# Kernel optimization log

Hardware: AMD Instinct MI355X
Metric: run time of the kernel (lower is better)

Reference implementation:

```python
import jax, jax.numpy as jnp
import numpy as np
import math

ALPHA, BETA, GAMMA = 12.0, 24.0, 96.0  # alpha=12, beta=2a, gamma=8a
PIX_PER_PATCH = 12.0                    # 200 // 16
HEADS = 8


def _bucket_ids(ct):
    # ct: (B,T,2) -> pairwise euclidean distance, trunc-divided by pix_per_patch
    d = ct[:, :, None, :] - ct[:, None, :, :]
    dist = jnp.trunc(jnp.sqrt(jnp.sum(d * d, axis=-1)) / PIX_PER_PATCH)
    absd = jnp.abs(dist)
    safe = jnp.maximum(absd, ALPHA)  # avoid log(0) in non-selected branch
    log_branch = jnp.sign(dist) * jnp.minimum(
        BETA, jnp.round(ALPHA + jnp.log(safe / ALPHA) / math.log(GAMMA / ALPHA) * (BETA - ALPHA)))
    # piecewise_index: identity (truncated to int) inside [-alpha, alpha], log-spaced outside
    idx = jnp.where(absd <= ALPHA, dist, log_branch).astype(jnp.int32) + int(BETA)
    return idx  # (B,T,T), values in [0, 2*beta]


def reference(x, ct, W_attn, b_attn, W_proj, b_proj, lut_bias):
    B, T, _ = x.shape
    H = HEADS
    n_embd = W_proj.shape[0]
    hd = n_embd // H
    idx = _bucket_ids(ct)

    qkv = x @ W_attn + b_attn                 # (B,T,3*n_embd)
    q, k, v = jnp.split(qkv, 3, axis=-1)
    q = q.reshape(B, T, H, hd).transpose(0, 2, 1, 3)  # (B,H,T,hd)
    k = k.reshape(B, T, H, hd).transpose(0, 2, 1, 3)
    v = v.reshape(B, T, H, hd).transpose(0, 2, 1, 3)

    att = jnp.einsum('bhtd,bhsd->bhts', q, k) / math.sqrt(hd)  # (B,H,T,T)
    # mask buffer is all-ones in the original, so masked_fill is a no-op.
    # Faithful to torch: gather (H, B*T*T) then raw row-major view to (B,H,T,T)
    rpe = lut_bias[:, idx.reshape(-1)].reshape(B, H, T, T)
    att = jax.nn.softmax(att + rpe, axis=-1)

    y = jnp.einsum('bhts,bhsd->bhtd', att, v)  # (B,H,T,hd)
    y = y.transpose(0, 2, 1, 3).reshape(B, T, n_embd)
    return y @ W_proj + b_proj


def setup_inputs() -> dict:
    B, T, IN_C, N_EMBD, NB = 16, 500, 512, 512, 49
    key = jax.random.key(0)
    ks = jax.random.split(key, 7)
    s = 0.02
    return {
        'x': jax.random.normal(ks[0], (B, T, IN_C), jnp.float32),
        'ct': jax.random.uniform(ks[1], (B, T, 2), jnp.float32) * 200.0,
        'W_attn': jax.random.normal(ks[2], (IN_C, 3 * N_EMBD), jnp.float32) * s,
        'b_attn': jax.random.normal(ks[3], (3 * N_EMBD,), jnp.float32) * s,
        'W_proj': jax.random.normal(ks[4], (N_EMBD, N_EMBD), jnp.float32) * s,
        'b_proj': jax.random.normal(ks[5], (N_EMBD,), jnp.float32) * s,
        'lut_bias': jax.random.normal(ks[6], (HEADS, NB), jnp.float32) * s,
    }
```

## Files before the change

### kernel.cpp

```cpp
#include <hip/hip_runtime.h>
#include <hip/hip_bf16.h>

typedef __bf16 bf16;
typedef __bf16 bf16x4 __attribute__((ext_vector_type(4)));
typedef __bf16 bf16x8 __attribute__((ext_vector_type(8)));
typedef float  f32x4  __attribute__((ext_vector_type(4)));

#define MFMA(a, b, c) __builtin_amdgcn_mfma_f32_16x16x32_bf16((a), (b), (c), 0, 0, 0)

__device__ __forceinline__ void async_ld16(void* l, const void* g) {
    __builtin_amdgcn_global_load_lds(
        (const __attribute__((address_space(1))) void*)g,
        (__attribute__((address_space(3))) void*)l, 16, 0, 0);
}


__global__ void cvt_f32_bf16(const float4* __restrict__ src, ushort4* __restrict__ dst, int n4) {
    for (int i = blockIdx.x * blockDim.x + threadIdx.x; i < n4; i += gridDim.x * blockDim.x) {
        float4 v = src[i];
        ushort4 o;
        o.x = (unsigned short)(__bfloat16_as_ushort(__float2bfloat16(v.x)));
        o.y = (unsigned short)(__bfloat16_as_ushort(__float2bfloat16(v.y)));
        o.z = (unsigned short)(__bfloat16_as_ushort(__float2bfloat16(v.z)));
        o.w = (unsigned short)(__bfloat16_as_ushort(__float2bfloat16(v.w)));
        dst[i] = o;
    }
}

__global__ void transpose_f32_bf16(const float* __restrict__ src, bf16* __restrict__ dst,
                                   int K, int N) {
    int i = blockIdx.x * 256 + threadIdx.x;
    if (i < K * N) {
        int k = i / N, n = i % N;
        dst[n * K + k] = (bf16)src[i];
    }
}

__global__ void pad_zero(bf16* __restrict__ xb, bf16* __restrict__ yb,
                         bf16* __restrict__ qb, bf16* __restrict__ kbuf,
                         bf16* __restrict__ vtb) {
    const bf16x8 z8 = {(bf16)0.f, (bf16)0.f, (bf16)0.f, (bf16)0.f,
                       (bf16)0.f, (bf16)0.f, (bf16)0.f, (bf16)0.f};
    const bf16x4 z4 = {(bf16)0.f, (bf16)0.f, (bf16)0.f, (bf16)0.f};
    int i = blockIdx.x * 256 + threadIdx.x;
    if (i < 4096) {
        *(bf16x8*)(xb + (size_t)8000 * 512 + i * 8) = z8;
    } else if (i < 8192) {
        *(bf16x8*)(yb + (size_t)8000 * 512 + (i - 4096) * 8) = z8;
    } else if (i < 20480) {
        int c = i - 8192;
        int bh = c / 96, rem = c % 96;
        int t = 500 + rem / 8, d8 = rem % 8;
        *(bf16x8*)(qb + (((size_t)bh * 512 + t) * 64) + d8 * 8) = z8;
    } else if (i < 32768) {
        int c = i - 20480;
        int bh = c / 96, rem = c % 96;
        int t = 500 + rem / 8, d8 = rem % 8;
        *(bf16x8*)(kbuf + (((size_t)bh * 512 + t) * 64) + d8 * 8) = z8;
    } else if (i < 40960) {
        int w = i - 32768;
        int bh = w >> 6, d = w & 63;
        bf16* base = vtb + ((size_t)bh * 64 + d) * 512 + 500;
        *(bf16x4*)base = z4;
        *(bf16x8*)(base + 4) = z8;
    }
}

__global__ void bucket_kernel(const float* __restrict__ ct, unsigned char* __restrict__ idx) {
    const int b = blockIdx.x >> 9;
    const int t = blockIdx.x & 511;
    const bool tv = (t < 500);
    float ctx = 0.f, cty = 0.f;
    if (tv) {
        ctx = ct[(b * 500 + t) * 2];
        cty = ct[(b * 500 + t) * 2 + 1];
    }
    const int s0 = threadIdx.x * 4;
    uchar4 o;
    unsigned char v[4];
#pragma unroll
    for (int j = 0; j < 4; j++) {
        int s = s0 + j;
        unsigned char r = 63;
        if (tv && s < 500) {
            float dx = ctx - ct[(b * 500 + s) * 2];
            float dy = cty - ct[(b * 500 + s) * 2 + 1];
            float dist = truncf(sqrtf(dx * dx + dy * dy) / 12.0f);
            int bi;
            if (dist <= 12.0f) {
                bi = (int)dist;
            } else {
                float lb = fminf(24.0f, rintf(12.0f + (logf(dist / 12.0f) * (1.0f / 2.0794415416798357f)) * 12.0f));
                bi = (int)lb;
            }
            r = (unsigned char)(bi + 24);
        }
        v[j] = r;
    }
    o.x = v[0]; o.y = v[1]; o.z = v[2]; o.w = v[3];
    *(uchar4*)(idx + ((size_t)blockIdx.x) * 512 + s0) = o;
}

template<int BN, int WGM, int WGN, int EPI>
__global__ __launch_bounds__(256) void gemm128(const bf16* __restrict__ A,
                                               const bf16* __restrict__ Bt,
                                               const float* __restrict__ bias,
                                               bf16* __restrict__ o_q,
                                               bf16* __restrict__ o_k,
                                               bf16* __restrict__ o_v,
                                               float* __restrict__ o_f) {
    constexpr int BM = 128, BK = 64, K = 512, NT = K / BK;
    constexpr int WM = BM / (WGM * 16);
    constexpr int WN = BN / (WGN * 16);
    constexpr int NA = BM * 8 / 256;
    constexpr int NB = BN * 8 / 256;
    constexpr int LD = (BM + BN) * BK;

    __shared__ __align__(1024) bf16 lds[2 * LD];

    const int lane = threadIdx.x & 63;
    const int wave = threadIdx.x >> 6;

    const int gdx = gridDim.x;
    const int nwg = gdx * gridDim.y;
    const int bid = blockIdx.y * gdx + blockIdx.x;
    const int qq = nwg >> 3, rr = nwg & 7;
    const int xcd = bid & 7, jj = bid >> 3;
    const int wg = (xcd < rr ? xcd * (qq + 1) : rr * (qq + 1) + (xcd - rr) * qq) + jj;
    const int m0 = (wg / gdx) * BM;
    const int n0 = (wg % gdx) * BN;

    const int wr = wave / WGN, wc = wave % WGN;
    const int r = lane & 15, g = lane >> 4;

    const bf16* pa[NA];
    const bf16* pb[NB];
    int loA[NA], loB[NB];
#pragma unroll
    for (int i = 0; i < NA; i++) {
        int cbase = i * 256 + wave * 64;
        int c = cbase + lane;
        int row = c >> 3, cb = (c & 7) * 16;
        pa[i] = A + (size_t)(m0 + row) * K + ((cb ^ ((row & 7) << 4)) >> 1);
        loA[i] = cbase * 8;
    }
#pragma unroll
    for (int i = 0; i < NB; i++) {
        int cbase = i * 256 + wave * 64;
        int c = cbase + lane;
        int row = c >> 3, cb = (c & 7) * 16;
        pb[i] = Bt + (size_t)(n0 + row) * K + ((cb ^ ((row & 7) << 4)) >> 1);
        loB[i] = cbase * 8;
    }

    f32x4 acc[WM][WN];
#pragma unroll
    for (int i = 0; i < WM; i++)
#pragma unroll
        for (int j = 0; j < WN; j++) acc[i][j] = (f32x4){0.f, 0.f, 0.f, 0.f};

    auto stage = [&](int buf, int kt) {
        bf16* la = lds + buf * LD;
        bf16* lb = la + BM * BK;
#pragma unroll
        for (int i = 0; i < NA; i++) async_ld16(la + loA[i], pa[i] + kt);
#pragma unroll
        for (int i = 0; i < NB; i++) async_ld16(lb + loB[i], pb[i] + kt);
    };

    stage(0, 0);
    int cur = 0;
#pragma unroll
    for (int t = 0; t < NT; t++) {
        if (t + 1 < NT) {
            stage(cur ^ 1, (t + 1) * BK);
            asm volatile("s_waitcnt vmcnt(%0)" ::"i"(NA + NB) : "memory");
        } else {
            asm volatile("s_waitcnt vmcnt(0)" ::: "memory");
        }
        __builtin_amdgcn_s_barrier();
        const bf16* la = lds + cur * LD;
        const bf16* lb = la + BM * BK;
#pragma unroll
        for (int kh = 0; kh < 2; kh++) {
            const int cb = kh * 64 + g * 16;
            bf16x8 af[WM], bfv[WN];
#pragma unroll
            for (int mf = 0; mf < WM; mf++) {
                int fr = wr * WM * 16 + mf * 16 + r;
                af[mf] = *(const bf16x8*)&la[fr * 64 + ((cb ^ ((fr & 7) << 4)) >> 1)];
            }
#pragma unroll
            for (int nf = 0; nf < WN; nf++) {
                int fr = wc * WN * 16 + nf * 16 + r;
                bfv[nf] = *(const bf16x8*)&lb[fr * 64 + ((cb ^ ((fr & 7) << 4)) >> 1)];
            }
#pragma unroll
            for (int mf = 0; mf < WM; mf++)
#pragma unroll
                for (int nf = 0; nf < WN; nf++)
                    acc[mf][nf] = MFMA(af[mf], bfv[nf], acc[mf][nf]);
        }
        asm volatile("" ::: "memory");
        __builtin_amdgcn_s_barrier();
        cur ^= 1;
    }

    if (EPI == 0) {
        const bool isv = (n0 >= 1024);
        bf16* tile = lds;
#pragma unroll
        for (int mf = 0; mf < WM; mf++)
#pragma unroll
            for (int nf = 0; nf < WN; nf++) {
                int nl = wc * WN * 16 + nf * 16 + r;
                float bv = bias[n0 + nl];
#pragma unroll
                for (int reg = 0; reg < 4; reg++) {
                    int ml = wr * WM * 16 + mf * 16 + g * 4 + reg;
                    bf16 val = (bf16)(acc[mf][nf][reg] + bv);
                    int byte = isv ? (nl * 256 + ((ml * 2) ^ ((nl & 7) << 4)))
                                   : (ml * 256 + ((nl * 2) ^ ((ml & 7) << 4)));
                    tile[byte >> 1] = val;
                }
            }
        __syncthreads();
        const int h0 = (n0 & 511) >> 6;
        if (!isv) {
            bf16* dst = (n0 < 512) ? o_q : o_k;
#pragma unroll
            for (int j = 0; j < 8; j++) {
                int seg = wave * 64 + j * 8 + (lane >> 3);
                int ml = seg >> 1, hp = seg & 1;
                int m = m0 + ml;
                if (m < 8000) {
                    int cb2 = (hp * 128 + (lane & 7) * 16) ^ ((ml & 7) << 4);
                    bf16x8 v8 = *(const bf16x8*)&tile[(ml * 256 + cb2) >> 1];
                    int b = m / 500, t = m - b * 500;
                    *(bf16x8*)&dst[(((size_t)(b * 8 + h0 + hp)) * 512 + t) * 64 + (lane & 7) * 8] = v8;
                }
            }
        } else {
#pragma unroll
            for (int j = 0; j < 8; j++) {
                int seg = wave * 64 + j * 8 + (lane >> 3);
                int nl = seg >> 1, mh = seg & 1;
                int mloc = mh * 64 + (lane & 7) * 8;
                int m = m0 + mloc;
                if (m < 8000) {
                    int cb2 = (mh * 128 + (lane & 7) * 16) ^ ((nl & 7) << 4);
                    bf16x8 v8 = *(const bf16x8*)&tile[(nl * 256 + cb2) >> 1];
                    int h = h0 + (nl >> 6), d = nl & 63;
                    int b0 = m / 500, b1 = (m + 7) / 500;
                    if (b0 == b1) {
                        int t = m - b0 * 500;
                        bf16* p = o_v + (((size_t)(b0 * 8 + h)) * 64 + d) * 512 + t;
                        if ((t & 7) == 0) {
                            *(bf16x8*)p = v8;
                        } else {
                            bf16x4 lo = {v8[0], v8[1], v8[2], v8[3]};
                            bf16x4 hi = {v8[4], v8[5], v8[6], v8[7]};
                            *(bf16x4*)p = lo;
                            *(bf16x4*)(p + 4) = hi;
                        }
                    } else {
#pragma unroll
                        for (int i = 0; i < 8; i++) {
                            int mi = m + i;
                            int bb = mi / 500, tt = mi - bb * 500;
                            o_v[(((size_t)(bb * 8 + h)) * 64 + d) * 512 + tt] = v8[i];
                        }
                    }
                }
            }
        }
    } else {
#pragma unroll
        for (int mf = 0; mf < WM; mf++) {
#pragma unroll
            for (int nf = 0; nf < WN; nf++) {
                int n = n0 + wc * WN * 16 + nf * 16 + r;
                float bv = bias[n];
#pragma unroll
                for (int reg = 0; reg < 4; reg++) {
                    int m = m0 + wr * WM * 16 + mf * 16 + g * 4 + reg;
                    if (m < 8000) o_f[(size_t)m * 512 + n] = acc[mf][nf][reg] + bv;
                }
            }
        }
    }
}

__global__ __launch_bounds__(256) void attn_kernel(const bf16* __restrict__ qb,
                                                   const bf16* __restrict__ kbuf,
                                                   const bf16* __restrict__ vtb,
                                                   const unsigned char* __restrict__ idxg,
                                                   const float* __restrict__ lut,
                                                   bf16* __restrict__ yb) {
    __shared__ __align__(1024) bf16 KT[2][4096];
    __shared__ __align__(1024) bf16 VT[2][4096];
    __shared__ float lut_s[64];
    __shared__ __align__(16) bf16 P[4][2][16][72];

    const int lane = threadIdx.x & 63;
    const int wave = threadIdx.x >> 6;
    const int tid = threadIdx.x;
    const int bid0 = blockIdx.x;
    const int wg = (bid0 & 7) * 64 + (bid0 >> 3);
    const int bh = wg >> 2;
    const int qt = wg & 3;
    const int b = bh >> 3;
    const int h = bh & 7;

    if (tid < 64)
        lut_s[tid] = (tid < 49) ? lut[h * 49 + tid] * 1.4426950408889634f : -1e30f;

    const int r = lane & 15;
    const int g = lane >> 4;
    const int ko = g << 3;
    const int rowbase = qt * 128 + wave * 32;

    bf16x8 qf[2][2];
#pragma unroll
    for (int c = 0; c < 2; c++) {
        const bf16* qp = qb + ((size_t)bh * 512 + rowbase + c * 16 + r) * 64 + ko;
        qf[c][0] = *(const bf16x8*)qp;
        qf[c][1] = *(const bf16x8*)(qp + 32);
    }

    const bf16* kbb = kbuf + (size_t)bh * 512 * 64;
    const bf16* vbb = vtb + (size_t)bh * 64 * 512;
    const unsigned char* ip0 = idxg + ((size_t)b * 512 + rowbase + r) * 512;
    const unsigned char* ip1 = ip0 + (size_t)16 * 512;

    const int c0 = tid, c1 = 256 + tid;
    const int kr0 = c0 >> 3, ks0 = (c0 & 7) * 16;
    const int kr1 = c1 >> 3, ks1 = (c1 & 7) * 16;
    const bf16* ksrc0 = kbb + (size_t)kr0 * 64 + ((ks0 ^ ((kr0 & 7) << 4)) >> 1);
    const bf16* ksrc1 = kbb + (size_t)kr1 * 64 + ((ks1 ^ ((kr1 & 7) << 4)) >> 1);
    const bf16* vsrc0 = vbb + (size_t)kr0 * 512 + ((ks0 ^ ((kr0 & 7) << 4)) >> 1);
    const bf16* vsrc1 = vbb + (size_t)kr1 * 512 + ((ks1 ^ ((kr1 & 7) << 4)) >> 1);

    auto stage = [&](int buf, int s0) {
        async_ld16(&KT[buf][c0 * 8], ksrc0 + (size_t)s0 * 64);
        async_ld16(&KT[buf][c1 * 8], ksrc1 + (size_t)s0 * 64);
        async_ld16(&VT[buf][c0 * 8], vsrc0 + s0);
        async_ld16(&VT[buf][c1 * 8], vsrc1 + s0);
    };

    unsigned int idb[2][2][4];
    auto ldidx = [&](int par, int s0) {
#pragma unroll
        for (int nf = 0; nf < 4; nf++) {
            idb[par][0][nf] = *(const unsigned int*)(ip0 + s0 + nf * 16 + (g << 2));
            idb[par][1][nf] = *(const unsigned int*)(ip1 + s0 + nf * 16 + (g << 2));
        }
    };

    f32x4 o[2][4];
#pragma unroll
    for (int c = 0; c < 2; c++)
#pragma unroll
        for (int i = 0; i < 4; i++) o[c][i] = (f32x4){0.f, 0.f, 0.f, 0.f};
    float lsum[2] = {0.f, 0.f};

    const float QS = 0.125f * 1.4426950408889634f;

    stage(0, 0);
    ldidx(0, 0);
#pragma unroll
    for (int ti = 0; ti < 8; ti++) {
        const int buf = ti & 1;
        const int s0 = ti * 64;
        if (ti < 7) {
            stage(buf ^ 1, s0 + 64);
            ldidx((ti + 1) & 1, s0 + 64);
            asm volatile("s_waitcnt vmcnt(12)" ::: "memory");
        } else {
            asm volatile("s_waitcnt vmcnt(0)" ::: "memory");
        }
        __builtin_amdgcn_s_barrier();
        f32x4 sa[2][4];
        __builtin_amdgcn_s_setprio(1);
#pragma unroll
        for (int nf = 0; nf < 4; nf++) {
            const int row = nf * 16 + r;
            const int swz = (row & 7) << 4;
            bf16x8 kf0 = *(const bf16x8*)&KT[buf][row * 64 + (((g * 16) ^ swz) >> 1)];
            bf16x8 kf1 = *(const bf16x8*)&KT[buf][row * 64 + (((g * 16 + 64) ^ swz) >> 1)];
            sa[0][nf] = MFMA(kf0, qf[0][0], ((f32x4){0.f, 0.f, 0.f, 0.f}));
            sa[0][nf] = MFMA(kf1, qf[0][1], sa[0][nf]);
            sa[1][nf] = MFMA(kf0, qf[1][0], ((f32x4){0.f, 0.f, 0.f, 0.f}));
            sa[1][nf] = MFMA(kf1, qf[1][1], sa[1][nf]);
        }
        __builtin_amdgcn_s_setprio(0);
#pragma unroll
        for (int c = 0; c < 2; c++) {
            float ts = 0.f;
#pragma unroll
            for (int nf = 0; nf < 4; nf++) {
                unsigned int u = idb[ti & 1][c][nf];
                float p0 = exp2f(fmaf(sa[c][nf][0], QS, lut_s[u & 255]));
                float p1 = exp2f(fmaf(sa[c][nf][1], QS, lut_s[(u >> 8) & 255]));
                float p2 = exp2f(fmaf(sa[c][nf][2], QS, lut_s[(u >> 16) & 255]));
                float p3 = exp2f(fmaf(sa[c][nf][3], QS, lut_s[u >> 24]));
                ts += (p0 + p1) + (p2 + p3);
                bf16x4 pk = {(bf16)p0, (bf16)p1, (bf16)p2, (bf16)p3};
                *(bf16x4*)&P[wave][c][r][nf * 16 + (g << 2)] = pk;
            }
            lsum[c] += ts;
        }
        bf16x8 pf00 = *(const bf16x8*)&P[wave][0][r][ko];
        bf16x8 pf01 = *(const bf16x8*)&P[wave][0][r][32 + ko];
        bf16x8 pf10 = *(const bf16x8*)&P[wave][1][r][ko];
        bf16x8 pf11 = *(const bf16x8*)&P[wave][1][r][32 + ko];
        __builtin_amdgcn_s_setprio(1);
#pragma unroll
        for (int nf = 0; nf < 4; nf++) {
            const int row = nf * 16 + r;
            const int swz = (row & 7) << 4;
            bf16x8 vf0 = *(const bf16x8*)&VT[buf][row * 64 + (((g * 16) ^ swz) >> 1)];
            bf16x8 vf1 = *(const bf16x8*)&VT[buf][row * 64 + (((g * 16 + 64) ^ swz) >> 1)];
            o[0][nf] = MFMA(pf00, vf0, o[0][nf]);
            o[0][nf] = MFMA(pf01, vf1, o[0][nf]);
            o[1][nf] = MFMA(pf10, vf0, o[1][nf]);
            o[1][nf] = MFMA(pf11, vf1, o[1][nf]);
        }
        __builtin_amdgcn_s_setprio(0);
        asm volatile("" ::: "memory");
        __builtin_amdgcn_s_barrier();
    }
#pragma unroll
    for (int c = 0; c < 2; c++) {
        float ls = lsum[c];
        ls += __shfl_xor(ls, 16);
        ls += __shfl_xor(ls, 32);
        float invl = 1.0f / ls;
#pragma unroll
        for (int reg = 0; reg < 4; reg++) {
            float il = __shfl(invl, (g << 2) + reg);
            int t = rowbase + c * 16 + (g << 2) + reg;
            if (t < 500) {
                bf16* yp = yb + ((size_t)(b * 500 + t)) * 512 + h * 64;
#pragma unroll
                for (int nf = 0; nf < 4; nf++) yp[nf * 16 + r] = (bf16)(o[c][nf][reg] * il);
            }
        }
    }
}

extern "C" void kernel_launch(void* const* d_in, const int* in_sizes, int n_in,
                              void* d_out, int out_size, void* d_ws, size_t ws_size,
                              hipStream_t stream) {
    const float* x     = (const float*)d_in[0];
    const float* ct    = (const float*)d_in[1];
    const float* Wattn = (const float*)d_in[2];
    const float* battn = (const float*)d_in[3];
    const float* Wproj = (const float*)d_in[4];
    const float* bproj = (const float*)d_in[5];
    const float* lut   = (const float*)d_in[6];
    float* out = (float*)d_out;

    char* w = (char*)d_ws;
    bf16* xb   = (bf16*)w;                w += (size_t)8064 * 512 * 2;
    bf16* Wa_t = (bf16*)w;                w += (size_t)1536 * 512 * 2;
    bf16* Wp_t = (bf16*)w;                w += (size_t)512 * 512 * 2;
    bf16* qb   = (bf16*)w;                w += (size_t)16 * 8 * 512 * 64 * 2;
    bf16* kbuf = (bf16*)w;                w += (size_t)16 * 8 * 512 * 64 * 2;
    bf16* vtb  = (bf16*)w;                w += (size_t)16 * 8 * 64 * 512 * 2;
    unsigned char* idxb = (unsigned char*)w; w += (size_t)16 * 512 * 512;
    bf16* yb   = (bf16*)w;                w += (size_t)8064 * 512 * 2;

    cvt_f32_bf16<<<dim3(2048), 256, 0, stream>>>((const float4*)x, (ushort4*)xb, (8000 * 512) / 4);
    transpose_f32_bf16<<<dim3((512 * 1536 + 255) / 256), 256, 0, stream>>>(Wattn, Wa_t, 512, 1536);
    transpose_f32_bf16<<<dim3((512 * 512 + 255) / 256), 256, 0, stream>>>(Wproj, Wp_t, 512, 512);
    pad_zero<<<dim3(160), 256, 0, stream>>>(xb, yb, qb, kbuf, vtb);
    bucket_kernel<<<dim3(16 * 512), 128, 0, stream>>>(ct, idxb);

    gemm128<128, 2, 2, 0><<<dim3(12, 63), 256, 0, stream>>>(xb, Wa_t, battn, qb, kbuf, vtb, nullptr);

    attn_kernel<<<dim3(512), 256, 0, stream>>>(qb, kbuf, vtb, idxb, lut, yb);

    gemm128<64, 4, 1, 1><<<dim3(8, 63), 256, 0, stream>>>(yb, Wp_t, bproj, nullptr, nullptr, nullptr, out);
}
```

Before: 93.02 us.

## Double KV tile to 128 keys and reorder barrier before prefetch in attention

```diff
diff --git a/kernel.cpp b/kernel.cpp
--- a/kernel.cpp
+++ b/kernel.cpp
@@ -297,8 +297,8 @@
                                                    const unsigned char* __restrict__ idxg,
                                                    const float* __restrict__ lut,
                                                    bf16* __restrict__ yb) {
-    __shared__ __align__(1024) bf16 KT[2][4096];
-    __shared__ __align__(1024) bf16 VT[2][4096];
+    __shared__ __align__(1024) bf16 KT[2][8192];
+    __shared__ __align__(1024) bf16 VT[2][8192];
     __shared__ float lut_s[64];
     __shared__ __align__(16) bf16 P[4][2][16][72];
 
@@ -330,31 +330,37 @@
 
     const bf16* kbb = kbuf + (size_t)bh * 512 * 64;
     const bf16* vbb = vtb + (size_t)bh * 64 * 512;
+
+    const bf16* ksrc[4];
+    const bf16* vsrc[4];
+    int loC[4];
+#pragma unroll
+    for (int i = 0; i < 4; i++) {
+        int c = i * 256 + tid;
+        loC[i] = c * 8;
+        int kr = c >> 3, ks = (c & 7) * 16;
+        ksrc[i] = kbb + (size_t)kr * 64 + ((ks ^ ((kr & 7) << 4)) >> 1);
+        int vr = c >> 4, vs = (c & 15) * 16;
+        vsrc[i] = vbb + (size_t)vr * 512 + ((vs ^ ((vr & 7) << 4)) >> 1);
+    }
+    auto stage = [&](int buf, int s0) {
+#pragma unroll
+        for (int i = 0; i < 4; i++) async_ld16(&KT[buf][loC[i]], ksrc[i] + (size_t)s0 * 64);
+#pragma unroll
+        for (int i = 0; i < 4; i++) async_ld16(&VT[buf][loC[i]], vsrc[i] + s0);
+    };
+
     const unsigned char* ip0 = idxg + ((size_t)b * 512 + rowbase + r) * 512;
     const unsigned char* ip1 = ip0 + (size_t)16 * 512;
-
-    const int c0 = tid, c1 = 256 + tid;
-    const int kr0 = c0 >> 3, ks0 = (c0 & 7) * 16;
-    const int kr1 = c1 >> 3, ks1 = (c1 & 7) * 16;
-    const bf16* ksrc0 = kbb + (size_t)kr0 * 64 + ((ks0 ^ ((kr0 & 7) << 4)) >> 1);
-    const bf16* ksrc1 = kbb + (size_t)kr1 * 64 + ((ks1 ^ ((kr1 & 7) << 4)) >> 1);
-    const bf16* vsrc0 = vbb + (size_t)kr0 * 512 + ((ks0 ^ ((kr0 & 7) << 4)) >> 1);
-    const bf16* vsrc1 = vbb + (size_t)kr1 * 512 + ((ks1 ^ ((kr1 & 7) << 4)) >> 1);
-
-    auto stage = [&](int buf, int s0) {
-        async_ld16(&KT[buf][c0 * 8], ksrc0 + (size_t)s0 * 64);
-        async_ld16(&KT[buf][c1 * 8], ksrc1 + (size_t)s0 * 64);
-        async_ld16(&VT[buf][c0 * 8], vsrc0 + s0);
-        async_ld16(&VT[buf][c1 * 8], vsrc1 + s0);
-    };
-
-    unsigned int idb[2][2][4];
+    unsigned int idb[2][2][2][4];
     auto ldidx = [&](int par, int s0) {
 #pragma unroll
-        for (int nf = 0; nf < 4; nf++) {
-            idb[par][0][nf] = *(const unsigned int*)(ip0 + s0 + nf * 16 + (g << 2));
-            idb[par][1][nf] = *(const unsigned int*)(ip1 + s0 + nf * 16 + (g << 2));
-        }
+        for (int sub = 0; sub < 2; sub++)
+#pragma unroll
+            for (int nf = 0; nf < 4; nf++) {
+                idb[par][sub][0][nf] = *(const unsigned int*)(ip0 + s0 + sub * 64 + nf * 16 + (g << 2));
+                idb[par][sub][1][nf] = *(const unsigned int*)(ip1 + s0 + sub * 64 + nf * 16 + (g << 2));
+            }
     };
 
     f32x4 o[2][4];
@@ -369,66 +375,65 @@
     stage(0, 0);
     ldidx(0, 0);
 #pragma unroll
-    for (int ti = 0; ti < 8; ti++) {
-        const int buf = ti & 1;
-        const int s0 = ti * 64;
-        if (ti < 7) {
-            stage(buf ^ 1, s0 + 64);
-            ldidx((ti + 1) & 1, s0 + 64);
-            asm volatile("s_waitcnt vmcnt(12)" ::: "memory");
-        } else {
-            asm volatile("s_waitcnt vmcnt(0)" ::: "memory");
-        }
+    for (int it = 0; it < 4; it++) {
+        const int buf = it & 1;
+        const int s0 = it * 128;
+        asm volatile("s_waitcnt vmcnt(0)" ::: "memory");
         __builtin_amdgcn_s_barrier();
-        f32x4 sa[2][4];
-        __builtin_amdgcn_s_setprio(1);
-#pragma unroll
-        for (int nf = 0; nf < 4; nf++) {
-            const int row = nf * 16 + r;
-            const int swz = (row & 7) << 4;
-            bf16x8 kf0 = *(const bf16x8*)&KT[buf][row * 64 + (((g * 16) ^ swz) >> 1)];
-            bf16x8 kf1 = *(const bf16x8*)&KT[buf][row * 64 + (((g * 16 + 64) ^ swz) >> 1)];
-            sa[0][nf] = MFMA(kf0, qf[0][0], ((f32x4){0.f, 0.f, 0.f, 0.f}));
-            sa[0][nf] = MFMA(kf1, qf[0][1], sa[0][nf]);
-            sa[1][nf] = MFMA(kf0, qf[1][0], ((f32x4){0.f, 0.f, 0.f, 0.f}));
-            sa[1][nf] = MFMA(kf1, qf[1][1], sa[1][nf]);
-        }
-        __builtin_amdgcn_s_setprio(0);
-#pragma unroll
-        for (int c = 0; c < 2; c++) {
-            float ts = 0.f;
+        if (it < 3) {
+            stage(buf ^ 1, s0 + 128);
+            ldidx((it + 1) & 1, s0 + 128);
+        }
+#pragma unroll
+        for (int sub = 0; sub < 2; sub++) {
+            f32x4 sa[2][4];
+            __builtin_amdgcn_s_setprio(1);
 #pragma unroll
             for (int nf = 0; nf < 4; nf++) {
-                unsigned int u = idb[ti & 1][c][nf];
-                float p0 = exp2f(fmaf(sa[c][nf][0], QS, lut_s[u & 255]));
-                float p1 = exp2f(fmaf(sa[c][nf][1], QS, lut_s[(u >> 8) & 255]));
-                float p2 = exp2f(fmaf(sa[c][nf][2], QS, lut_s[(u >> 16) & 255]));
-                float p3 = exp2f(fmaf(sa[c][nf][3], QS, lut_s[u >> 24]));
-                ts += (p0 + p1) + (p2 + p3);
-                bf16x4 pk = {(bf16)p0, (bf16)p1, (bf16)p2, (bf16)p3};
-                *(bf16x4*)&P[wave][c][r][nf * 16 + (g << 2)] = pk;
-            }
-            lsum[c] += ts;
-        }
-        bf16x8 pf00 = *(const bf16x8*)&P[wave][0][r][ko];
-        bf16x8 pf01 = *(const bf16x8*)&P[wave][0][r][32 + ko];
-        bf16x8 pf10 = *(const bf16x8*)&P[wave][1][r][ko];
-        bf16x8 pf11 = *(const bf16x8*)&P[wave][1][r][32 + ko];
-        __builtin_amdgcn_s_setprio(1);
-#pragma unroll
-        for (int nf = 0; nf < 4; nf++) {
-            const int row = nf * 16 + r;
-            const int swz = (row & 7) << 4;
-            bf16x8 vf0 = *(const bf16x8*)&VT[buf][row * 64 + (((g * 16) ^ swz) >> 1)];
-            bf16x8 vf1 = *(const bf16x8*)&VT[buf][row * 64 + (((g * 16 + 64) ^ swz) >> 1)];
-            o[0][nf] = MFMA(pf00, vf0, o[0][nf]);
-            o[0][nf] = MFMA(pf01, vf1, o[0][nf]);
-            o[1][nf] = MFMA(pf10, vf0, o[1][nf]);
-            o[1][nf] = MFMA(pf11, vf1, o[1][nf]);
-        }
-        __builtin_amdgcn_s_setprio(0);
-        asm volatile("" ::: "memory");
-        __builtin_amdgcn_s_barrier();
+                const int row = sub * 64 + nf * 16 + r;
+                const int swz = (row & 7) << 4;
+                bf16x8 kf0 = *(const bf16x8*)&KT[buf][row * 64 + (((g * 16) ^ swz) >> 1)];
+                bf16x8 kf1 = *(const bf16x8*)&KT[buf][row * 64 + (((g * 16 + 64) ^ swz) >> 1)];
+                sa[0][nf] = MFMA(kf0, qf[0][0], ((f32x4){0.f, 0.f, 0.f, 0.f}));
+                sa[0][nf] = MFMA(kf1, qf[0][1], sa[0][nf]);
+                sa[1][nf] = MFMA(kf0, qf[1][0], ((f32x4){0.f, 0.f, 0.f, 0.f}));
+                sa[1][nf] = MFMA(kf1, qf[1][1], sa[1][nf]);
+            }
+            __builtin_amdgcn_s_setprio(0);
+#pragma unroll
+            for (int c = 0; c < 2; c++) {
+                float ts = 0.f;
+#pragma unroll
+                for (int nf = 0; nf < 4; nf++) {
+                    unsigned int u = idb[it & 1][sub][c][nf];
+                    float p0 = exp2f(fmaf(sa[c][nf][0], QS, lut_s[u & 255]));
+                    float p1 = exp2f(fmaf(sa[c][nf][1], QS, lut_s[(u >> 8) & 255]));
+                    float p2 = exp2f(fmaf(sa[c][nf][2], QS, lut_s[(u >> 16) & 255]));
+                    float p3 = exp2f(fmaf(sa[c][nf][3], QS, lut_s[u >> 24]));
+                    ts += (p0 + p1) + (p2 + p3);
+                    bf16x4 pk = {(bf16)p0, (bf16)p1, (bf16)p2, (bf16)p3};
+                    *(bf16x4*)&P[wave][c][r][nf * 16 + (g << 2)] = pk;
+                }
+                lsum[c] += ts;
+            }
+            bf16x8 pf00 = *(const bf16x8*)&P[wave][0][r][ko];
+            bf16x8 pf01 = *(const bf16x8*)&P[wave][0][r][32 + ko];
+            bf16x8 pf10 = *(const bf16x8*)&P[wave][1][r][ko];
+            bf16x8 pf11 = *(const bf16x8*)&P[wave][1][r][32 + ko];
+            __builtin_amdgcn_s_setprio(1);
+#pragma unroll
+            for (int nf = 0; nf < 4; nf++) {
+                const int row = nf * 16 + r;
+                const int swz = (row & 7) << 4;
+                bf16x8 vf0 = *(const bf16x8*)&VT[buf][row * 128 + (((sub * 128 + g * 16) ^ swz) >> 1)];
+                bf16x8 vf1 = *(const bf16x8*)&VT[buf][row * 128 + (((sub * 128 + g * 16 + 64) ^ swz) >> 1)];
+                o[0][nf] = MFMA(pf00, vf0, o[0][nf]);
+                o[0][nf] = MFMA(pf01, vf1, o[0][nf]);
+                o[1][nf] = MFMA(pf10, vf0, o[1][nf]);
+                o[1][nf] = MFMA(pf11, vf1, o[1][nf]);
+            }
+            __builtin_amdgcn_s_setprio(0);
+        }
     }
 #pragma unroll
     for (int c = 0; c < 2; c++) {
```

Result: slower. 102.9 us (+10.7%).
